# Kernel tuning notes

Hardware: AMD Instinct MI355X
Metric: run time of the kernel (lower is better)

The kernel has to match this reference:

```python
import jax, jax.numpy as jnp
import numpy as np

B, S, D, H = 2, 2048, 1024, 16
DK = D // H


def setup_inputs() -> dict:
    key = jax.random.key(0)
    ks = jax.random.split(key, 7)
    q = jax.random.normal(ks[0], (B, S, D), dtype=jnp.float32)
    k = jax.random.normal(ks[1], (B, S, D), dtype=jnp.float32)
    v = jax.random.normal(ks[2], (B, S, D), dtype=jnp.float32)
    # causal mask: mask==0 positions get -1e9 before softmax
    mask = jnp.tril(jnp.ones((S, S), dtype=jnp.int32))[None, None, :, :]
    scale = 0.02
    w_q = jax.random.normal(ks[3], (D, D), dtype=jnp.float32) * scale
    w_k = jax.random.normal(ks[4], (D, D), dtype=jnp.float32) * scale
    w_v = jax.random.normal(ks[5], (D, D), dtype=jnp.float32) * scale
    w_o = jax.random.normal(ks[6], (D, D), dtype=jnp.float32) * scale
    return {"q": q, "k": k, "v": v, "mask": mask,
            "w_q": w_q, "w_k": w_k, "w_v": w_v, "w_o": w_o}


def reference(q, k, v, mask, w_q, w_k, w_v, w_o):
    # nn.Linear(bias=False): x @ W.T
    query = q @ w_q.T  # [B,S,D]
    key = k @ w_k.T
    value = v @ w_v.T
    # split heads -> [B,H,S,DK]
    query = query.reshape(B, S, H, DK).transpose(0, 2, 1, 3)
    key = key.reshape(B, S, H, DK).transpose(0, 2, 1, 3)
    value = value.reshape(B, S, H, DK).transpose(0, 2, 1, 3)
    scores = jnp.einsum('bhqd,bhkd->bhqk', query, key) / jnp.sqrt(
        jnp.asarray(DK, dtype=query.dtype))
    scores = jnp.where(mask == 0, jnp.asarray(-1e9, scores.dtype), scores)
    attn = jax.nn.softmax(scores, axis=-1)  # dropout p=0.0 -> identity
    x = jnp.einsum('bhqk,bhkd->bhqd', attn, value)  # [B,H,S,DK]
    x = x.transpose(0, 2, 1, 3).reshape(B, S, D)
    return x @ w_o.T
```

## Files before the change

### kernel.cpp

```cpp
#include <hip/hip_runtime.h>

typedef __attribute__((ext_vector_type(8))) short short8;
typedef __attribute__((ext_vector_type(4))) float f32x4;

#define DEVI static __device__ __forceinline__

constexpr int BB = 2, SS = 2048, DD = 1024, HH = 16, DKK = 64;
constexpr size_t QN = (size_t)BB * SS * DD;
constexpr size_t WN = (size_t)DD * DD;

constexpr size_t OFF_WQ = 3 * QN;
constexpr size_t OFF_WO = OFF_WQ + 3 * WN;
constexpr size_t OFF_QM = OFF_WQ + 4 * WN;
constexpr size_t OFF_KM = OFF_QM + QN;
constexpr size_t OFF_VM = OFF_QM + 2 * QN;
constexpr size_t OFF_XC = OFF_QM + 3 * QN;

DEVI unsigned short f2bf(float f) {
  unsigned int u = __float_as_uint(f);
  u = (u + 0x7fffu + ((u >> 16) & 1u)) >> 16;
  return (unsigned short)u;
}

DEVI f32x4 fzero() { f32x4 z = {0.f, 0.f, 0.f, 0.f}; return z; }

DEVI void gld16(const void* g, void* l) {
  __builtin_amdgcn_global_load_lds((__attribute__((address_space(1))) void*)g,
                                   (__attribute__((address_space(3))) void*)l,
                                   16, 0, 0);
}

DEVI short8 mk8u(unsigned int a, unsigned int b, unsigned int c, unsigned int d) {
  union { short8 s; unsigned int u[4]; } x;
  x.u[0] = a; x.u[1] = b; x.u[2] = c; x.u[3] = d;
  return x.s;
}

DEVI short8 mk8q(unsigned long long lo, unsigned long long hi) {
  union { short8 s; unsigned long long q[2]; } x;
  x.q[0] = lo; x.q[1] = hi;
  return x.s;
}

DEVI unsigned int pkbf(float a, float b) {
  return __builtin_amdgcn_perm(__float_as_uint(b), __float_as_uint(a), 0x07060302u);
}

#define VMBAR(N) asm volatile("s_waitcnt vmcnt(" #N ")\n\ts_barrier" ::: "memory")
#define LGKM0                                      \
  do {                                             \
    asm volatile("s_waitcnt lgkmcnt(0)" ::: "memory"); \
    __builtin_amdgcn_sched_barrier(0);             \
  } while (0)

__global__ __launch_bounds__(256) void convert_all(
    const float* __restrict__ q, const float* __restrict__ k,
    const float* __restrict__ v, const float* __restrict__ wq,
    const float* __restrict__ wk, const float* __restrict__ wv,
    const float* __restrict__ wo, unsigned short* __restrict__ ws) {
  size_t t = (size_t)blockIdx.x * 256 + threadIdx.x;
  size_t e = t * 4;
  const float* src;
  size_t base, idx;
  if (e < 3 * QN) {
    size_t a = e >> 22;
    idx = e & (QN - 1);
    src = (a == 0) ? q : (a == 1) ? k : v;
    base = a * QN;
  } else {
    size_t r = e - 3 * QN;
    size_t a = r >> 20;
    idx = r & (WN - 1);
    src = (a == 0) ? wq : (a == 1) ? wk : (a == 2) ? wv : wo;
    base = 3 * QN + a * WN;
  }
  float4 f = *(const float4*)(src + idx);
  ushort4 o;
  o.x = f2bf(f.x); o.y = f2bf(f.y); o.z = f2bf(f.z); o.w = f2bf(f.w);
  *(ushort4*)(ws + base + idx) = o;
}

__global__ __launch_bounds__(512, 2) void proj_gemm(unsigned short* __restrict__ ws) {
  __shared__ unsigned short lds[65536];
  const int tid = threadIdx.x;
  const int w = tid >> 6, l = tid & 63;
  const int lr = l & 15, qd = l >> 4, l7 = l & 7, l3 = l >> 3;
  const int wr = w >> 2, wc = w & 3;

  const int orig = blockIdx.x;
  const int swz = (orig & 7) * 24 + (orig >> 3);
  const int mt = swz >> 2, nt = swz & 3;
  const int z = mt >> 4;
  const int m0 = (mt & 15) * 256, n0 = nt * 256;

  const unsigned short* Ab = ws + (size_t)z * QN;
  const unsigned short* Wb = ws + OFF_WQ + (size_t)z * WN;
  unsigned short* O = ws + OFF_QM + (size_t)z * QN;

  f32x4 acc[8][4];
#pragma unroll
  for (int i = 0; i < 8; ++i)
#pragma unroll
    for (int j = 0; j < 4; ++j) acc[i][j] = fzero();

  auto stage = [&](int buf, int ab, int h, int kt) {
    const unsigned short* src = ab ? Wb : Ab;
    const int rc0 = (ab ? n0 : m0) + h * 128 + w * 8 + l3;
    const int kofs = kt * 64 + ((l7 ^ l3) * 8);
    unsigned short* d = &lds[buf * 32768 + ab * 16384 + h * 8192 + w * 512];
#pragma unroll
    for (int u = 0; u < 2; ++u)
      gld16(src + (size_t)(rc0 + u * 64) * DD + kofs, d + u * 4096);
  };
  auto rdA = [&](int buf, int fi, int ks) -> short8 {
    const int rg = (fi * 2 + wr) * 16 + lr;
    const int c2 = (ks * 4 + qd) ^ l7;
    return *(const short8*)&lds[buf * 32768 + rg * 64 + c2 * 8];
  };
  auto rdB = [&](int buf, int fj, int ks) -> short8 {
    const int rg = (fj * 4 + wc) * 16 + lr;
    const int c2 = (ks * 4 + qd) ^ l7;
    return *(const short8*)&lds[buf * 32768 + 16384 + rg * 64 + c2 * 8];
  };

  stage(0, 0, 0, 0);
  stage(0, 1, 0, 0);
  stage(0, 1, 1, 0);
  stage(0, 0, 1, 0);

  constexpr int NT = DD / 64;
#pragma unroll 1
  for (int t = 0; t < NT; ++t) {
    const int rb = t & 1, wb = rb ^ 1;
    const bool g = (t + 1 < NT);
    short8 af[4][2], bf[2][2], bh[2][2];

    VMBAR(4);
    if (g) stage(wb, 0, 0, t + 1);
#pragma unroll
    for (int mi = 0; mi < 4; ++mi)
#pragma unroll
      for (int ks = 0; ks < 2; ++ks) af[mi][ks] = rdA(rb, mi, ks);
#pragma unroll
    for (int nj = 0; nj < 2; ++nj)
#pragma unroll
      for (int ks = 0; ks < 2; ++ks) bf[nj][ks] = rdB(rb, nj, ks);
    LGKM0;
    __builtin_amdgcn_s_setprio(1);
#pragma unroll
    for (int mi = 0; mi < 4; ++mi)
#pragma unroll
      for (int nj = 0; nj < 2; ++nj)
#pragma unroll
        for (int ks = 0; ks < 2; ++ks)
          acc[mi][nj] = __builtin_amdgcn_mfma_f32_16x16x32_bf16(
              af[mi][ks], bf[nj][ks], acc[mi][nj], 0, 0, 0);
    __builtin_amdgcn_s_setprio(0);

    if (g) { VMBAR(4); } else { VMBAR(2); }
    if (g) stage(wb, 1, 0, t + 1);
#pragma unroll
    for (int nj = 0; nj < 2; ++nj)
#pragma unroll
      for (int ks = 0; ks < 2; ++ks) bh[nj][ks] = rdB(rb, 2 + nj, ks);
    LGKM0;
    __builtin_amdgcn_s_setprio(1);
#pragma unroll
    for (int mi = 0; mi < 4; ++mi)
#pragma unroll
      for (int nj = 0; nj < 2; ++nj)
#pragma unroll
        for (int ks = 0; ks < 2; ++ks)
          acc[mi][2 + nj] = __builtin_amdgcn_mfma_f32_16x16x32_bf16(
              af[mi][ks], bh[nj][ks], acc[mi][2 + nj], 0, 0, 0);
    __builtin_amdgcn_s_setprio(0);

    if (g) { VMBAR(4); } else { VMBAR(0); }
    if (g) stage(wb, 1, 1, t + 1);
#pragma unroll
    for (int mi = 0; mi < 4; ++mi)
#pragma unroll
      for (int ks = 0; ks < 2; ++ks) af[mi][ks] = rdA(rb, 4 + mi, ks);
    LGKM0;
    __builtin_amdgcn_s_setprio(1);
#pragma unroll
    for (int mi = 0; mi < 4; ++mi)
#pragma unroll
      for (int nj = 0; nj < 2; ++nj)
#pragma unroll
        for (int ks = 0; ks < 2; ++ks)
          acc[4 + mi][nj] = __builtin_amdgcn_mfma_f32_16x16x32_bf16(
              af[mi][ks], bf[nj][ks], acc[4 + mi][nj], 0, 0, 0);
    __builtin_amdgcn_s_setprio(0);

    if (g) stage(wb, 0, 1, t + 1);
    __builtin_amdgcn_s_setprio(1);
#pragma unroll
    for (int mi = 0; mi < 4; ++mi)
#pragma unroll
      for (int nj = 0; nj < 2; ++nj)
#pragma unroll
        for (int ks = 0; ks < 2; ++ks)
          acc[4 + mi][2 + nj] = __builtin_amdgcn_mfma_f32_16x16x32_bf16(
              af[mi][ks], bh[nj][ks], acc[4 + mi][2 + nj], 0, 0, 0);
    __builtin_amdgcn_s_setprio(0);
  }

  if (z == 2) {
#pragma unroll
    for (int fi = 0; fi < 8; ++fi)
#pragma unroll
      for (int fj = 0; fj < 4; ++fj) {
        const int n = n0 + (fj * 4 + wc) * 16 + lr;
        const int h = n >> 6, dk = n & 63;
        const int m = m0 + (fi * 2 + wr) * 16 + qd * 4;
        const int b = m >> 11, s = m & 2047;
        ushort4 pk;
        pk.x = f2bf(acc[fi][fj][0]); pk.y = f2bf(acc[fi][fj][1]);
        pk.z = f2bf(acc[fi][fj][2]); pk.w = f2bf(acc[fi][fj][3]);
        *(ushort4*)&O[((size_t)(b * HH + h) * DKK + dk) * SS + s] = pk;
      }
  } else {
#pragma unroll
    for (int fi = 0; fi < 8; ++fi)
#pragma unroll
      for (int fj = 0; fj < 4; ++fj) {
        const int n = n0 + (fj * 4 + wc) * 16 + lr;
        const int h = n >> 6, dk = n & 63;
#pragma unroll
        for (int i = 0; i < 4; ++i) {
          const int m = m0 + (fi * 2 + wr) * 16 + qd * 4 + i;
          const int b = m >> 11, s = m & 2047;
          O[((size_t)(b * HH + h) * SS + s) * DKK + dk] = f2bf(acc[fi][fj][i]);
        }
      }
  }
}

__global__ __launch_bounds__(512) void flash_attn(
    const unsigned short* __restrict__ Qm, const unsigned short* __restrict__ Km,
    const unsigned short* __restrict__ Vt, unsigned short* __restrict__ Xc) {
  __shared__ unsigned short Kl[2][4096];
  __shared__ unsigned short Vl[2][4096];
  const int head = blockIdx.x, py = blockIdx.y, b = blockIdx.z;
  const int p = b ? 15 - py : py;
  const int tid = threadIdx.x, w = tid >> 6, l = tid & 63, lr = l & 15, qd = l >> 4;
  const int slr = lr ^ ((lr >> 3) << 2);
  const size_t bh = (size_t)(b * HH + head);
  const unsigned short* Qb = Qm + bh * SS * DKK;
  const unsigned short* Kb = Km + bh * SS * DKK;
  const unsigned short* Vb = Vt + bh * DKK * SS;

  const bool heavy = (w < 4);
  const int qt = heavy ? (31 - p) : p;
  const int nkv = 32 - p;
  const int qrow = qt * 64 + (w & 3) * 16 + lr;

  const int s0 = heavy ? w : (w - 4);
  const int s1 = s0 + 4;
  const int loOff = ((qd >> 1) * 16 + slr) * 8 + (qd & 1) * 4;
  const int hiOff = ((2 + (qd >> 1)) * 16 + slr) * 8 + (qd & 1) * 4;

  short8 qf0 = *(const short8*)&Qb[(size_t)qrow * DKK + qd * 8];
  short8 qf1 = *(const short8*)&Qb[(size_t)qrow * DKK + 32 + qd * 8];

  f32x4 o[4];
#pragma unroll
  for (int i = 0; i < 4; ++i) o[i] = fzero();
  float ll = 0.f;
  const float c1 = 0.18033688011112042f;
  const float mc = 8.0f * c1;

  {
    if (heavy) {
      gld16(&Kb[(size_t)((s0 >> 1) * 16 + lr) * DKK + (s0 & 1) * 32 + qd * 8],
            &Kl[0][s0 * 512]);
      gld16(&Kb[(size_t)((s1 >> 1) * 16 + lr) * DKK + (s1 & 1) * 32 + qd * 8],
            &Kl[0][s1 * 512]);
    } else {
      gld16(&Vb[(size_t)((s0 >> 1) * 16 + slr) * SS + (s0 & 1) * 32 + qd * 8],
            &Vl[0][s0 * 512]);
      gld16(&Vb[(size_t)((s1 >> 1) * 16 + slr) * SS + (s1 & 1) * 32 + qd * 8],
            &Vl[0][s1 * 512]);
    }
  }

#pragma unroll 1
  for (int kv = 0; kv < nkv; ++kv) {
    __syncthreads();
    const int cur = kv & 1;
    if (kv + 1 < nkv) {
      const int kv0n = (kv + 1) * 64;
      if (heavy) {
        gld16(&Kb[(size_t)(kv0n + (s0 >> 1) * 16 + lr) * DKK + (s0 & 1) * 32 + qd * 8],
              &Kl[cur ^ 1][s0 * 512]);
        gld16(&Kb[(size_t)(kv0n + (s1 >> 1) * 16 + lr) * DKK + (s1 & 1) * 32 + qd * 8],
              &Kl[cur ^ 1][s1 * 512]);
      } else {
        gld16(&Vb[(size_t)((s0 >> 1) * 16 + slr) * SS + kv0n + (s0 & 1) * 32 + qd * 8],
              &Vl[cur ^ 1][s0 * 512]);
        gld16(&Vb[(size_t)((s1 >> 1) * 16 + slr) * SS + kv0n + (s1 & 1) * 32 + qd * 8],
              &Vl[cur ^ 1][s1 * 512]);
      }
    }

    if (kv <= qt) {
      const int kv0 = kv * 64;
      f32x4 sc[4];
#pragma unroll
      for (int nt = 0; nt < 4; ++nt) {
        short8 kf0 = *(const short8*)&Kl[cur][(nt * 2 + 0) * 512 + l * 8];
        short8 kf1 = *(const short8*)&Kl[cur][(nt * 2 + 1) * 512 + l * 8];
        f32x4 zz = fzero();
        zz = __builtin_amdgcn_mfma_f32_16x16x32_bf16(kf0, qf0, zz, 0, 0, 0);
        sc[nt] = __builtin_amdgcn_mfma_f32_16x16x32_bf16(kf1, qf1, zz, 0, 0, 0);
      }
      if (kv == qt) {
#pragma unroll
        for (int nt = 0; nt < 4; ++nt)
#pragma unroll
          for (int i = 0; i < 4; ++i) {
            const int kvi = kv0 + nt * 16 + qd * 4 + i;
            if (kvi > qrow) sc[nt][i] = -3e38f;
          }
      }

#pragma unroll
      for (int nt = 0; nt < 4; ++nt)
#pragma unroll
        for (int i = 0; i < 4; ++i) {
          const float pp = exp2f(fmaf(sc[nt][i], c1, -mc));
          sc[nt][i] = pp;
          ll += pp;
        }

      unsigned int pd[4][2];
#pragma unroll
      for (int f = 0; f < 4; ++f) {
        pd[f][0] = pkbf(sc[f][0], sc[f][1]);
        pd[f][1] = pkbf(sc[f][2], sc[f][3]);
      }

#pragma unroll
      for (int kh = 0; kh < 2; ++kh) {
        short8 bfr = mk8u(pd[2 * kh][0], pd[2 * kh][1],
                          pd[2 * kh + 1][0], pd[2 * kh + 1][1]);
#pragma unroll
        for (int mt = 0; mt < 4; ++mt) {
          const int sbase = (mt * 2 + kh) * 512;
          const unsigned long long lo =
              *(const unsigned long long*)&Vl[cur][sbase + loOff];
          const unsigned long long hi =
              *(const unsigned long long*)&Vl[cur][sbase + hiOff];
          o[mt] = __builtin_amdgcn_mfma_f32_16x16x32_bf16(mk8q(lo, hi), bfr,
                                                          o[mt], 0, 0, 0);
        }
      }
    }
  }

  ll += __shfl_xor(ll, 16);
  ll += __shfl_xor(ll, 32);

  const float inv = 1.0f / ll;
  unsigned short* Xr = Xc + ((size_t)b * SS + qrow) * DD + (size_t)head * DKK;
#pragma unroll
  for (int mt = 0; mt < 4; ++mt)
#pragma unroll
    for (int i = 0; i < 4; ++i)
      Xr[mt * 16 + qd * 4 + i] = f2bf(o[mt][i] * inv);
}

__global__ __launch_bounds__(256, 2) void out_gemm(
    const unsigned short* __restrict__ Xc, const unsigned short* __restrict__ Wo,
    float* __restrict__ out) {
  __shared__ unsigned short lds[32768];
  const int tid = threadIdx.x;
  const int w = tid >> 6, l = tid & 63;
  const int lr = l & 15, qd = l >> 4, l7 = l & 7, l3 = l >> 3;
  const int wr = w >> 1, wc = w & 1;
  const int m0 = blockIdx.x * 128, n0 = blockIdx.y * 128;

  f32x4 acc[4][4];
#pragma unroll
  for (int i = 0; i < 4; ++i)
#pragma unroll
    for (int j = 0; j < 4; ++j) acc[i][j] = fzero();

  auto stage = [&](int buf, int ab, int h, int kt) {
    const unsigned short* src = ab ? Wo : Xc;
    const int rc0 = (ab ? n0 : m0) + h * 64 + w * 8 + l3;
    const int kofs = kt * 64 + ((l7 ^ l3) * 8);
    unsigned short* d = &lds[buf * 16384 + ab * 8192 + h * 4096 + w * 512];
#pragma unroll
    for (int u = 0; u < 2; ++u)
      gld16(src + (size_t)(rc0 + u * 32) * DD + kofs, d + u * 2048);
  };
  auto rdA = [&](int buf, int mf, int ks) -> short8 {
    const int rg = mf * 16 + lr;
    const int c2 = (ks * 4 + qd) ^ l7;
    return *(const short8*)&lds[buf * 16384 + rg * 64 + c2 * 8];
  };
  auto rdB = [&](int buf, int nf, int ks) -> short8 {
    const int rg = nf * 16 + lr;
    const int c2 = (ks * 4 + qd) ^ l7;
    return *(const short8*)&lds[buf * 16384 + 8192 + rg * 64 + c2 * 8];
  };

  stage(0, 0, 0, 0);
  stage(0, 1, 0, 0);
  stage(0, 1, 1, 0);
  stage(0, 0, 1, 0);

  constexpr int NT = DD / 64;
#pragma unroll 1
  for (int t = 0; t < NT; ++t) {
    const int rb = t & 1, wb = rb ^ 1;
    const bool g = (t + 1 < NT);
    short8 af[2][2], bf[2][2], bh[2][2];

    VMBAR(4);
    if (g) stage(wb, 0, 0, t + 1);
#pragma unroll
    for (int mi = 0; mi < 2; ++mi)
#pragma unroll
      for (int ks = 0; ks < 2; ++ks) af[mi][ks] = rdA(rb, mi * 2 + wr, ks);
#pragma unroll
    for (int nj = 0; nj < 2; ++nj)
#pragma unroll
      for (int ks = 0; ks < 2; ++ks) bf[nj][ks] = rdB(rb, nj * 2 + wc, ks);
    LGKM0;
    __builtin_amdgcn_s_setprio(1);
#pragma unroll
    for (int mi = 0; mi < 2; ++mi)
#pragma unroll
      for (int nj = 0; nj < 2; ++nj)
#pragma unroll
        for (int ks = 0; ks < 2; ++ks)
          acc[mi][nj] = __builtin_amdgcn_mfma_f32_16x16x32_bf16(
              af[mi][ks], bf[nj][ks], acc[mi][nj], 0, 0, 0);
    __builtin_amdgcn_s_setprio(0);

    if (g) { VMBAR(4); } else { VMBAR(2); }
    if (g) stage(wb, 1, 0, t + 1);
#pragma unroll
    for (int nj = 0; nj < 2; ++nj)
#pragma unroll
      for (int ks = 0; ks < 2; ++ks) bh[nj][ks] = rdB(rb, (2 + nj) * 2 + wc, ks);
    LGKM0;
    __builtin_amdgcn_s_setprio(1);
#pragma unroll
    for (int mi = 0; mi < 2; ++mi)
#pragma unroll
      for (int nj = 0; nj < 2; ++nj)
#pragma unroll
        for (int ks = 0; ks < 2; ++ks)
          acc[mi][2 + nj] = __builtin_amdgcn_mfma_f32_16x16x32_bf16(
              af[mi][ks], bh[nj][ks], acc[mi][2 + nj], 0, 0, 0);
    __builtin_amdgcn_s_setprio(0);

    if (g) { VMBAR(4); } else { VMBAR(0); }
    if (g) stage(wb, 1, 1, t + 1);
#pragma unroll
    for (int mi = 0; mi < 2; ++mi)
#pragma unroll
      for (int ks = 0; ks < 2; ++ks) af[mi][ks] = rdA(rb, (2 + mi) * 2 + wr, ks);
    LGKM0;
    __builtin_amdgcn_s_setprio(1);
#pragma unroll
    for (int mi = 0; mi < 2; ++mi)
#pragma unroll
      for (int nj = 0; nj < 2; ++nj)
#pragma unroll
        for (int ks = 0; ks < 2; ++ks)
          acc[2 + mi][nj] = __builtin_amdgcn_mfma_f32_16x16x32_bf16(
              af[mi][ks], bf[nj][ks], acc[2 + mi][nj], 0, 0, 0);
    __builtin_amdgcn_s_setprio(0);

    if (g) stage(wb, 0, 1, t + 1);
    __builtin_amdgcn_s_setprio(1);
#pragma unroll
    for (int mi = 0; mi < 2; ++mi)
#pragma unroll
      for (int nj = 0; nj < 2; ++nj)
#pragma unroll
        for (int ks = 0; ks < 2; ++ks)
          acc[2 + mi][2 + nj] = __builtin_amdgcn_mfma_f32_16x16x32_bf16(
              af[mi][ks], bh[nj][ks], acc[2 + mi][2 + nj], 0, 0, 0);
    __builtin_amdgcn_s_setprio(0);
  }

#pragma unroll
  for (int a = 0; a < 4; ++a)
#pragma unroll
    for (int c = 0; c < 4; ++c) {
      const int n = n0 + (c * 2 + wc) * 16 + lr;
#pragma unroll
      for (int i = 0; i < 4; ++i) {
        const int m = m0 + (a * 2 + wr) * 16 + qd * 4 + i;
        out[(size_t)m * DD + n] = acc[a][c][i];
      }
    }
}

extern "C" void kernel_launch(void* const* d_in, const int* in_sizes, int n_in,
                              void* d_out, int out_size, void* d_ws, size_t ws_size,
                              hipStream_t stream) {
  (void)in_sizes; (void)n_in; (void)out_size; (void)ws_size;
  const float* q  = (const float*)d_in[0];
  const float* k  = (const float*)d_in[1];
  const float* v  = (const float*)d_in[2];
  const float* wq = (const float*)d_in[4];
  const float* wk = (const float*)d_in[5];
  const float* wv = (const float*)d_in[6];
  const float* wo = (const float*)d_in[7];
  unsigned short* ws = (unsigned short*)d_ws;
  float* out = (float*)d_out;

  convert_all<<<dim3(16384), dim3(256), 0, stream>>>(q, k, v, wq, wk, wv, wo, ws);
  proj_gemm<<<dim3(192), dim3(512), 0, stream>>>(ws);
  flash_attn<<<dim3(16, 16, 2), dim3(512), 0, stream>>>(ws + OFF_QM, ws + OFF_KM,
                                                        ws + OFF_VM, ws + OFF_XC);
  out_gemm<<<dim3(32, 8), dim3(256), 0, stream>>>(ws + OFF_XC, ws + OFF_WO, out);
}
```

Measured before the change: 215.6 us.

## Stage two KV tiles per barrier in flash attention loop

The flash attention loop now loads and processes two 64-row KV tiles per iteration, with double-buffered shared memory enlarged to hold both. This halves the number of __syncthreads barriers and puts larger prefetch batches in flight per step. The cost is doubled LDS use (64KB per block), which may limit occupancy, plus a longer unrolled body.

```diff
diff --git a/kernel.cpp b/kernel.cpp
--- a/kernel.cpp
+++ b/kernel.cpp
@@ -240,8 +240,8 @@
 __global__ __launch_bounds__(512) void flash_attn(
     const unsigned short* __restrict__ Qm, const unsigned short* __restrict__ Km,
     const unsigned short* __restrict__ Vt, unsigned short* __restrict__ Xc) {
-  __shared__ unsigned short Kl[2][4096];
-  __shared__ unsigned short Vl[2][4096];
+  __shared__ unsigned short Kl[2][8192];
+  __shared__ unsigned short Vl[2][8192];
   const int head = blockIdx.x, py = blockIdx.y, b = blockIdx.z;
   const int p = b ? 15 - py : py;
   const int tid = threadIdx.x, w = tid >> 6, l = tid & 63, lr = l & 15, qd = l >> 4;
@@ -261,6 +261,23 @@
   const int loOff = ((qd >> 1) * 16 + slr) * 8 + (qd & 1) * 4;
   const int hiOff = ((2 + (qd >> 1)) * 16 + slr) * 8 + (qd & 1) * 4;
 
+  auto stK = [&](int buf, int kvt) {
+    const size_t r0 = (size_t)kvt * 64;
+    unsigned short* d = &Kl[buf][(kvt & 1) * 4096];
+    gld16(&Kb[(r0 + (s0 >> 1) * 16 + lr) * DKK + (s0 & 1) * 32 + qd * 8],
+          d + s0 * 512);
+    gld16(&Kb[(r0 + (s1 >> 1) * 16 + lr) * DKK + (s1 & 1) * 32 + qd * 8],
+          d + s1 * 512);
+  };
+  auto stV = [&](int buf, int kvt) {
+    const size_t c0 = (size_t)kvt * 64;
+    unsigned short* d = &Vl[buf][(kvt & 1) * 4096];
+    gld16(&Vb[(size_t)((s0 >> 1) * 16 + slr) * SS + c0 + (s0 & 1) * 32 + qd * 8],
+          d + s0 * 512);
+    gld16(&Vb[(size_t)((s1 >> 1) * 16 + slr) * SS + c0 + (s1 & 1) * 32 + qd * 8],
+          d + s1 * 512);
+  };
+
   short8 qf0 = *(const short8*)&Qb[(size_t)qrow * DKK + qd * 8];
   short8 qf1 = *(const short8*)&Qb[(size_t)qrow * DKK + 32 + qd * 8];
 
@@ -272,88 +289,82 @@
   const float mc = 8.0f * c1;
 
   {
-    if (heavy) {
-      gld16(&Kb[(size_t)((s0 >> 1) * 16 + lr) * DKK + (s0 & 1) * 32 + qd * 8],
-            &Kl[0][s0 * 512]);
-      gld16(&Kb[(size_t)((s1 >> 1) * 16 + lr) * DKK + (s1 & 1) * 32 + qd * 8],
-            &Kl[0][s1 * 512]);
-    } else {
-      gld16(&Vb[(size_t)((s0 >> 1) * 16 + slr) * SS + (s0 & 1) * 32 + qd * 8],
-            &Vl[0][s0 * 512]);
-      gld16(&Vb[(size_t)((s1 >> 1) * 16 + slr) * SS + (s1 & 1) * 32 + qd * 8],
-            &Vl[0][s1 * 512]);
-    }
+    if (heavy) { stK(0, 0); stK(0, 1); }
+    else       { stV(0, 0); stV(0, 1); }
   }
 
+  const int nit = (nkv + 1) >> 1;
 #pragma unroll 1
-  for (int kv = 0; kv < nkv; ++kv) {
+  for (int it = 0; it < nit; ++it) {
     __syncthreads();
-    const int cur = kv & 1;
-    if (kv + 1 < nkv) {
-      const int kv0n = (kv + 1) * 64;
+    const int cur = it & 1;
+    if (it + 1 < nit) {
+      const int t0 = 2 * (it + 1), t1 = t0 + 1;
       if (heavy) {
-        gld16(&Kb[(size_t)(kv0n + (s0 >> 1) * 16 + lr) * DKK + (s0 & 1) * 32 + qd * 8],
-              &Kl[cur ^ 1][s0 * 512]);
-        gld16(&Kb[(size_t)(kv0n + (s1 >> 1) * 16 + lr) * DKK + (s1 & 1) * 32 + qd * 8],
-              &Kl[cur ^ 1][s1 * 512]);
+        stK(cur ^ 1, t0);
+        if (t1 < nkv) stK(cur ^ 1, t1);
       } else {
-        gld16(&Vb[(size_t)((s0 >> 1) * 16 + slr) * SS + kv0n + (s0 & 1) * 32 + qd * 8],
-              &Vl[cur ^ 1][s0 * 512]);
-        gld16(&Vb[(size_t)((s1 >> 1) * 16 + slr) * SS + kv0n + (s1 & 1) * 32 + qd * 8],
-              &Vl[cur ^ 1][s1 * 512]);
+        stV(cur ^ 1, t0);
+        if (t1 < nkv) stV(cur ^ 1, t1);
       }
     }
 
-    if (kv <= qt) {
-      const int kv0 = kv * 64;
-      f32x4 sc[4];
-#pragma unroll
-      for (int nt = 0; nt < 4; ++nt) {
-        short8 kf0 = *(const short8*)&Kl[cur][(nt * 2 + 0) * 512 + l * 8];
-        short8 kf1 = *(const short8*)&Kl[cur][(nt * 2 + 1) * 512 + l * 8];
-        f32x4 zz = fzero();
-        zz = __builtin_amdgcn_mfma_f32_16x16x32_bf16(kf0, qf0, zz, 0, 0, 0);
-        sc[nt] = __builtin_amdgcn_mfma_f32_16x16x32_bf16(kf1, qf1, zz, 0, 0, 0);
-      }
-      if (kv == qt) {
+#pragma unroll
+    for (int s = 0; s < 2; ++s) {
+      const int kvt = 2 * it + s;
+      if (kvt <= qt) {
+        const int kv0 = kvt * 64;
+        const unsigned short* Kc = &Kl[cur][s * 4096];
+        const unsigned short* Vc = &Vl[cur][s * 4096];
+        f32x4 sc[4];
+#pragma unroll
+        for (int nt = 0; nt < 4; ++nt) {
+          short8 kf0 = *(const short8*)&Kc[(nt * 2 + 0) * 512 + l * 8];
+          short8 kf1 = *(const short8*)&Kc[(nt * 2 + 1) * 512 + l * 8];
+          f32x4 zz = fzero();
+          zz = __builtin_amdgcn_mfma_f32_16x16x32_bf16(kf0, qf0, zz, 0, 0, 0);
+          sc[nt] = __builtin_amdgcn_mfma_f32_16x16x32_bf16(kf1, qf1, zz, 0, 0, 0);
+        }
+        if (kvt == qt) {
+#pragma unroll
+          for (int nt = 0; nt < 4; ++nt)
+#pragma unroll
+            for (int i = 0; i < 4; ++i) {
+              const int kvi = kv0 + nt * 16 + qd * 4 + i;
+              if (kvi > qrow) sc[nt][i] = -3e38f;
+            }
+        }
+
 #pragma unroll
         for (int nt = 0; nt < 4; ++nt)
 #pragma unroll
           for (int i = 0; i < 4; ++i) {
-            const int kvi = kv0 + nt * 16 + qd * 4 + i;
-            if (kvi > qrow) sc[nt][i] = -3e38f;
+            const float pp = exp2f(fmaf(sc[nt][i], c1, -mc));
+            sc[nt][i] = pp;
+            ll += pp;
           }
-      }
-
-#pragma unroll
-      for (int nt = 0; nt < 4; ++nt)
-#pragma unroll
-        for (int i = 0; i < 4; ++i) {
-          const float pp = exp2f(fmaf(sc[nt][i], c1, -mc));
-          sc[nt][i] = pp;
-          ll += pp;
+
+        unsigned int pd[4][2];
+#pragma unroll
+        for (int f = 0; f < 4; ++f) {
+          pd[f][0] = pkbf(sc[f][0], sc[f][1]);
+          pd[f][1] = pkbf(sc[f][2], sc[f][3]);
         }
 
-      unsigned int pd[4][2];
-#pragma unroll
-      for (int f = 0; f < 4; ++f) {
-        pd[f][0] = pkbf(sc[f][0], sc[f][1]);
-        pd[f][1] = pkbf(sc[f][2], sc[f][3]);
-      }
-
-#pragma unroll
-      for (int kh = 0; kh < 2; ++kh) {
-        short8 bfr = mk8u(pd[2 * kh][0], pd[2 * kh][1],
-                          pd[2 * kh + 1][0], pd[2 * kh + 1][1]);
-#pragma unroll
-        for (int mt = 0; mt < 4; ++mt) {
-          const int sbase = (mt * 2 + kh) * 512;
-          const unsigned long long lo =
-              *(const unsigned long long*)&Vl[cur][sbase + loOff];
-          const unsigned long long hi =
-              *(const unsigned long long*)&Vl[cur][sbase + hiOff];
-          o[mt] = __builtin_amdgcn_mfma_f32_16x16x32_bf16(mk8q(lo, hi), bfr,
-                                                          o[mt], 0, 0, 0);
+#pragma unroll
+        for (int kh = 0; kh < 2; ++kh) {
+          short8 bfr = mk8u(pd[2 * kh][0], pd[2 * kh][1],
+                            pd[2 * kh + 1][0], pd[2 * kh + 1][1]);
+#pragma unroll
+          for (int mt = 0; mt < 4; ++mt) {
+            const int sbase = (mt * 2 + kh) * 512;
+            const unsigned long long lo =
+                *(const unsigned long long*)&Vc[sbase + loOff];
+            const unsigned long long hi =
+                *(const unsigned long long*)&Vc[sbase + hiOff];
+            o[mt] = __builtin_amdgcn_mfma_f32_16x16x32_bf16(mk8q(lo, hi), bfr,
+                                                            o[mt], 0, 0, 0);
+          }
         }
       }
     }
```

After: 217.4 us. About the same (+0.9%).

## Load K and V fragments directly from global memory instead of LDS staging

Applied to the files above, without the earlier changes.

Removes the double-buffered shared-memory staging of K and V tiles along with the per-iteration block barrier. Each wave now reads its MFMA operands straight from global memory through per-lane pointers, and loops only over its own causal range. This removes LDS traffic and synchronisation, and lets the light and heavy waves run independently. In exchange, every wave fetches K/V itself through the cache instead of sharing one staged copy, and there is no explicit prefetch to hide load latency.

```diff
diff --git a/kernel.cpp b/kernel.cpp
--- a/kernel.cpp
+++ b/kernel.cpp
@@ -240,12 +240,9 @@
 __global__ __launch_bounds__(512) void flash_attn(
     const unsigned short* __restrict__ Qm, const unsigned short* __restrict__ Km,
     const unsigned short* __restrict__ Vt, unsigned short* __restrict__ Xc) {
-  __shared__ unsigned short Kl[2][4096];
-  __shared__ unsigned short Vl[2][4096];
   const int head = blockIdx.x, py = blockIdx.y, b = blockIdx.z;
   const int p = b ? 15 - py : py;
   const int tid = threadIdx.x, w = tid >> 6, l = tid & 63, lr = l & 15, qd = l >> 4;
-  const int slr = lr ^ ((lr >> 3) << 2);
   const size_t bh = (size_t)(b * HH + head);
   const unsigned short* Qb = Qm + bh * SS * DKK;
   const unsigned short* Kb = Km + bh * SS * DKK;
@@ -253,16 +250,17 @@
 
   const bool heavy = (w < 4);
   const int qt = heavy ? (31 - p) : p;
-  const int nkv = 32 - p;
   const int qrow = qt * 64 + (w & 3) * 16 + lr;
-
-  const int s0 = heavy ? w : (w - 4);
-  const int s1 = s0 + 4;
-  const int loOff = ((qd >> 1) * 16 + slr) * 8 + (qd & 1) * 4;
-  const int hiOff = ((2 + (qd >> 1)) * 16 + slr) * 8 + (qd & 1) * 4;
 
   short8 qf0 = *(const short8*)&Qb[(size_t)qrow * DKK + qd * 8];
   short8 qf1 = *(const short8*)&Qb[(size_t)qrow * DKK + 32 + qd * 8];
+
+  const unsigned short* kp = Kb + (size_t)lr * DKK + qd * 8;
+  const int cq = (qd >> 1) * 8 + (qd & 1) * 4;
+  const unsigned short* vp[4];
+#pragma unroll
+  for (int mt = 0; mt < 4; ++mt)
+    vp[mt] = Vb + (size_t)(mt * 16 + lr) * SS + cq;
 
   f32x4 o[4];
 #pragma unroll
@@ -271,92 +269,67 @@
   const float c1 = 0.18033688011112042f;
   const float mc = 8.0f * c1;
 
-  {
-    if (heavy) {
-      gld16(&Kb[(size_t)((s0 >> 1) * 16 + lr) * DKK + (s0 & 1) * 32 + qd * 8],
-            &Kl[0][s0 * 512]);
-      gld16(&Kb[(size_t)((s1 >> 1) * 16 + lr) * DKK + (s1 & 1) * 32 + qd * 8],
-            &Kl[0][s1 * 512]);
-    } else {
-      gld16(&Vb[(size_t)((s0 >> 1) * 16 + slr) * SS + (s0 & 1) * 32 + qd * 8],
-            &Vl[0][s0 * 512]);
-      gld16(&Vb[(size_t)((s1 >> 1) * 16 + slr) * SS + (s1 & 1) * 32 + qd * 8],
-            &Vl[0][s1 * 512]);
-    }
-  }
-
 #pragma unroll 1
-  for (int kv = 0; kv < nkv; ++kv) {
-    __syncthreads();
-    const int cur = kv & 1;
-    if (kv + 1 < nkv) {
-      const int kv0n = (kv + 1) * 64;
-      if (heavy) {
-        gld16(&Kb[(size_t)(kv0n + (s0 >> 1) * 16 + lr) * DKK + (s0 & 1) * 32 + qd * 8],
-              &Kl[cur ^ 1][s0 * 512]);
-        gld16(&Kb[(size_t)(kv0n + (s1 >> 1) * 16 + lr) * DKK + (s1 & 1) * 32 + qd * 8],
-              &Kl[cur ^ 1][s1 * 512]);
-      } else {
-        gld16(&Vb[(size_t)((s0 >> 1) * 16 + slr) * SS + kv0n + (s0 & 1) * 32 + qd * 8],
-              &Vl[cur ^ 1][s0 * 512]);
-        gld16(&Vb[(size_t)((s1 >> 1) * 16 + slr) * SS + kv0n + (s1 & 1) * 32 + qd * 8],
-              &Vl[cur ^ 1][s1 * 512]);
+  for (int kv = 0; kv <= qt; ++kv) {
+    short8 kf[4][2];
+#pragma unroll
+    for (int nt = 0; nt < 4; ++nt) {
+      kf[nt][0] = *(const short8*)(kp + nt * 16 * DKK);
+      kf[nt][1] = *(const short8*)(kp + nt * 16 * DKK + 32);
+    }
+
+    f32x4 sc[4];
+#pragma unroll
+    for (int nt = 0; nt < 4; ++nt) {
+      f32x4 zz = fzero();
+      zz = __builtin_amdgcn_mfma_f32_16x16x32_bf16(kf[nt][0], qf0, zz, 0, 0, 0);
+      sc[nt] = __builtin_amdgcn_mfma_f32_16x16x32_bf16(kf[nt][1], qf1, zz, 0, 0, 0);
+    }
+    if (kv == qt) {
+      const int kv0 = kv * 64;
+#pragma unroll
+      for (int nt = 0; nt < 4; ++nt)
+#pragma unroll
+        for (int i = 0; i < 4; ++i) {
+          const int kvi = kv0 + nt * 16 + qd * 4 + i;
+          if (kvi > qrow) sc[nt][i] = -3e38f;
+        }
+    }
+
+#pragma unroll
+    for (int nt = 0; nt < 4; ++nt)
+#pragma unroll
+      for (int i = 0; i < 4; ++i) {
+        const float pp = exp2f(fmaf(sc[nt][i], c1, -mc));
+        sc[nt][i] = pp;
+        ll += pp;
       }
-    }
-
-    if (kv <= qt) {
-      const int kv0 = kv * 64;
-      f32x4 sc[4];
-#pragma unroll
-      for (int nt = 0; nt < 4; ++nt) {
-        short8 kf0 = *(const short8*)&Kl[cur][(nt * 2 + 0) * 512 + l * 8];
-        short8 kf1 = *(const short8*)&Kl[cur][(nt * 2 + 1) * 512 + l * 8];
-        f32x4 zz = fzero();
-        zz = __builtin_amdgcn_mfma_f32_16x16x32_bf16(kf0, qf0, zz, 0, 0, 0);
-        sc[nt] = __builtin_amdgcn_mfma_f32_16x16x32_bf16(kf1, qf1, zz, 0, 0, 0);
+
+    unsigned int pd[4][2];
+#pragma unroll
+    for (int f = 0; f < 4; ++f) {
+      pd[f][0] = pkbf(sc[f][0], sc[f][1]);
+      pd[f][1] = pkbf(sc[f][2], sc[f][3]);
+    }
+
+#pragma unroll
+    for (int kh = 0; kh < 2; ++kh) {
+      short8 bfr = mk8u(pd[2 * kh][0], pd[2 * kh][1],
+                        pd[2 * kh + 1][0], pd[2 * kh + 1][1]);
+#pragma unroll
+      for (int mt = 0; mt < 4; ++mt) {
+        const unsigned long long lo =
+            *(const unsigned long long*)(vp[mt] + kh * 32);
+        const unsigned long long hi =
+            *(const unsigned long long*)(vp[mt] + kh * 32 + 16);
+        o[mt] = __builtin_amdgcn_mfma_f32_16x16x32_bf16(mk8q(lo, hi), bfr,
+                                                        o[mt], 0, 0, 0);
       }
-      if (kv == qt) {
-#pragma unroll
-        for (int nt = 0; nt < 4; ++nt)
-#pragma unroll
-          for (int i = 0; i < 4; ++i) {
-            const int kvi = kv0 + nt * 16 + qd * 4 + i;
-            if (kvi > qrow) sc[nt][i] = -3e38f;
-          }
-      }
-
-#pragma unroll
-      for (int nt = 0; nt < 4; ++nt)
-#pragma unroll
-        for (int i = 0; i < 4; ++i) {
-          const float pp = exp2f(fmaf(sc[nt][i], c1, -mc));
-          sc[nt][i] = pp;
-          ll += pp;
-        }
-
-      unsigned int pd[4][2];
-#pragma unroll
-      for (int f = 0; f < 4; ++f) {
-        pd[f][0] = pkbf(sc[f][0], sc[f][1]);
-        pd[f][1] = pkbf(sc[f][2], sc[f][3]);
-      }
-
-#pragma unroll
-      for (int kh = 0; kh < 2; ++kh) {
-        short8 bfr = mk8u(pd[2 * kh][0], pd[2 * kh][1],
-                          pd[2 * kh + 1][0], pd[2 * kh + 1][1]);
-#pragma unroll
-        for (int mt = 0; mt < 4; ++mt) {
-          const int sbase = (mt * 2 + kh) * 512;
-          const unsigned long long lo =
-              *(const unsigned long long*)&Vl[cur][sbase + loOff];
-          const unsigned long long hi =
-              *(const unsigned long long*)&Vl[cur][sbase + hiOff];
-          o[mt] = __builtin_amdgcn_mfma_f32_16x16x32_bf16(mk8q(lo, hi), bfr,
-                                                          o[mt], 0, 0, 0);
-        }
-      }
-    }
+    }
+
+    kp += 64 * DKK;
+#pragma unroll
+    for (int mt = 0; mt < 4; ++mt) vp[mt] += 64;
   }
 
   ll += __shfl_xor(ll, 16);
```

Result: slower. 349.2 us (+62.0%).
